# Kernel optimization log

Measured on AMD Instinct MI355X. Metric: run time of the kernel, lower is better.

The kernel has to match this reference:

```python
import jax, jax.numpy as jnp
import numpy as np
from jax import lax

N_EXPERTS = 256
N_GROUP = 8
TOPK_GROUP = 4
TOP_K = 8
AUX_ALPHA = 0.001


def setup_inputs() -> dict:
    key = jax.random.key(0)
    k1, k2 = jax.random.split(key)
    hidden_states = jax.random.normal(k1, (16384, 2048), dtype=jnp.float32)
    weight = jax.random.normal(k2, (N_EXPERTS, 2048), dtype=jnp.float32) * 0.02
    return {"hidden_states": hidden_states, "weight": weight}


def reference(hidden_states, weight):
    n_tokens = hidden_states.shape[0]
    group_size = N_EXPERTS // N_GROUP  # 32

    # gating logits: [N, E]
    logits = jnp.einsum('nh,eh->ne', hidden_states, weight)

    # group-restricted top-k: [N, G, group_size] -> top TOPK_GROUP per group
    group_logits = logits.reshape(n_tokens, N_GROUP, group_size)
    gw, gi = lax.top_k(group_logits, TOPK_GROUP)          # [N, G, tg]
    gw = gw.reshape(n_tokens, N_GROUP * TOPK_GROUP)
    gi = gi.reshape(n_tokens, N_GROUP * TOPK_GROUP)

    # global top-k over the pooled group winners
    topk_weights, ti = lax.top_k(gw, TOP_K)               # [N, K]
    selected_group = ti // TOPK_GROUP
    expert_in_group = jnp.take_along_axis(gi, ti, axis=1)
    topk_idx = selected_group * group_size + expert_in_group  # [N, K]

    # norm_topk_prob=True
    topk_weights = topk_weights / (jnp.sum(topk_weights, axis=-1, keepdims=True) + 1e-20)

    # auxiliary load-balancing loss (training path)
    expert_mask = jax.nn.one_hot(topk_idx.reshape(-1), N_EXPERTS, dtype=jnp.float32)
    expert_counts = expert_mask.mean(axis=0)              # [E]
    expert_probs = jax.nn.softmax(logits, axis=-1).mean(axis=0)  # [E]
    aux_loss = jnp.sum(expert_counts * expert_probs) * AUX_ALPHA

    return topk_idx, topk_weights, aux_loss
```

## Files before the change

kernel.cpp:

```cpp
#include <hip/hip_runtime.h>
#include <math.h>

#define NTOK 16384
#define KD   2048
#define NE   256
#define NCHUNK16 128
#define NCHUNK   64
#define CHUNK_DW 4096
#define TM 32
#define SL 257
#define SA 260

typedef float f32x2 __attribute__((ext_vector_type(2)));

__device__ __forceinline__ f32x2 pk_mul_lo(f32x2 a, f32x2 b) {
    f32x2 d;
    asm("v_pk_mul_f32 %0, %1, %2 op_sel:[0,0] op_sel_hi:[1,0]"
        : "=v"(d) : "v"(a), "v"(b));
    return d;
}
__device__ __forceinline__ f32x2 pk_mul_hi(f32x2 a, f32x2 b) {
    f32x2 d;
    asm("v_pk_mul_f32 %0, %1, %2 op_sel:[0,1] op_sel_hi:[1,1]"
        : "=v"(d) : "v"(a), "v"(b));
    return d;
}
__device__ __forceinline__ f32x2 pk_add(f32x2 a, f32x2 b) {
    f32x2 d;
    asm("v_pk_add_f32 %0, %1, %2" : "=v"(d) : "v"(a), "v"(b));
    return d;
}

__global__ __launch_bounds__(256) void transform_kernel(
    const float* __restrict__ wgt, float* __restrict__ Bt)
{
    const int c    = blockIdx.x >> 2;
    const int qt   = blockIdx.x & 3;
    const int slot = qt * 256 + threadIdx.x;
    const int s    = slot >> 6;
    const int lane = slot & 63;
    const int em   = lane >> 2;
    const int l    = lane & 3;
    const int e    = (s >> 1) * 32 + (s & 1) * 16 + em;
    const float* src = wgt + (size_t)e * KD + 16 * c + l;
    float4 v = make_float4(src[0], src[4], src[8], src[12]);
    *(float4*)(Bt + (size_t)c * CHUNK_DW + slot * 4) = v;
}

typedef __attribute__((address_space(1))) const void GV;
typedef __attribute__((address_space(3))) void LV;
__device__ __forceinline__ void gld_lds16(const float* g, float* l) {
    __builtin_amdgcn_global_load_lds((GV*)g, (LV*)l, 16, 0, 0);
}

__global__ __launch_bounds__(512, 4) void gate_kernel(
    const float* __restrict__ hid, const float* __restrict__ Bt,
    float* __restrict__ out, float* __restrict__ cnt, float* __restrict__ prb)
{
    __shared__ union { float bs[2][2 * CHUNK_DW]; float ls[TM][SL]; } sh;
    __shared__ float As2[2][4][SA];
    __shared__ float maxS[TM], sumS[TM], invS[TM];

    const int tid  = threadIdx.x;
    const int l    = tid & 3;
    const int eg   = (tid >> 2) & 31;
    const int tg   = tid >> 7;
    const int t0   = blockIdx.x * TM;
    const int lane = tid & 63;
    const int w    = tid >> 6;
    const int h    = w & 1;

    f32x2 acc2[4][8];
#pragma unroll
    for (int i = 0; i < 4; ++i)
#pragma unroll
        for (int j = 0; j < 8; ++j) acc2[i][j] = (f32x2){0.f, 0.f};

    const bool aact = (lane < 32);
    const int  at   = w * 4 + (lane >> 3);
    const int  aq   = lane & 7;
    float av[4];

    auto stageA_load = [&](int c) {
        if (aact)
            *(float4*)av = *(const float4*)(hid + (size_t)(t0 + at) * KD + 32 * c + 4 * aq);
    };
    auto stageA_write = [&](int buf) {
        if (aact) {
            const int base = (at >> 1) * 16 + aq * 2 + (at & 1);
#pragma unroll
            for (int ll = 0; ll < 4; ++ll)
                As2[buf][ll][base] = av[ll];
        }
    };
    auto stageB = [&](int c, int buf) {
        const float* src = Bt + (size_t)(2 * c) * CHUNK_DW + tid * 4;
        float* dst = &sh.bs[buf][tid * 4];
#pragma unroll
        for (int s = 0; s < 4; ++s)
            gld_lds16(src + s * 2048, dst + s * 2048);
    };

    stageA_load(0);
    stageB(0, 0);
    stageA_write(0);
    int cur = 0;

#pragma unroll 1
    for (int c = 0; c < NCHUNK; ++c) {
        __syncthreads();
        const int nxt = cur ^ 1;
        if (c + 1 < NCHUNK) { stageA_load(c + 1); stageB(c + 1, nxt); }

#pragma unroll
        for (int j16 = 0; j16 < 2; ++j16) {
            float4 a0[4], a1[4];
#pragma unroll
            for (int tp = 0; tp < 4; ++tp) {
                const float* ap = &As2[cur][l][(tg * 4 + tp) * 16 + j16 * 8];
                a0[tp] = *(const float4*)(ap);
                a1[tp] = *(const float4*)(ap + 4);
            }
#pragma unroll
            for (int j = 0; j < 8; ++j) {
                const float4 b = *(const float4*)
                    &sh.bs[cur][j16 * CHUNK_DW + ((j * 2 + h) << 8) + (lane << 2)];
                const f32x2 b01 = (f32x2){b.x, b.y};
                const f32x2 b23 = (f32x2){b.z, b.w};
#pragma unroll
                for (int tp = 0; tp < 4; ++tp) {
                    const f32x2 aQ0 = (f32x2){a0[tp].x, a0[tp].y};
                    const f32x2 aQ1 = (f32x2){a0[tp].z, a0[tp].w};
                    const f32x2 aQ2 = (f32x2){a1[tp].x, a1[tp].y};
                    const f32x2 aQ3 = (f32x2){a1[tp].z, a1[tp].w};
                    f32x2 s = acc2[tp][j];
                    s = pk_add(pk_mul_hi(aQ3, b23), s);
                    s = pk_add(pk_mul_lo(aQ2, b23), s);
                    s = pk_add(pk_mul_hi(aQ1, b01), s);
                    s = pk_add(pk_mul_lo(aQ0, b01), s);
                    acc2[tp][j] = s;
                }
            }
        }
        if (c + 1 < NCHUNK) stageA_write(nxt);
        cur = nxt;
    }

    __syncthreads();
#pragma unroll
    for (int tp = 0; tp < 4; ++tp)
#pragma unroll
        for (int j = 0; j < 8; ++j) {
            float sx = acc2[tp][j].x, sy = acc2[tp][j].y;
            sx = __fadd_rn(sx, __shfl_xor(sx, 1));
            sx = __fadd_rn(sx, __shfl_xor(sx, 2));
            sy = __fadd_rn(sy, __shfl_xor(sy, 1));
            sy = __fadd_rn(sy, __shfl_xor(sy, 2));
            if (l == 0) {
                sh.ls[tg * 8 + 2 * tp][eg + 32 * j]     = sx;
                sh.ls[tg * 8 + 2 * tp + 1][eg + 32 * j] = sy;
            }
        }
    if (tid < TM) sumS[tid] = 0.f;
    __syncthreads();

    if (tid < TM) {
        const float* lr = &sh.ls[tid][0];
        float tv[8]; int ti[8];
#pragma unroll
        for (int j = 0; j < 8; ++j) { tv[j] = -1e30f; ti[j] = 0; }
        float rowmax = -1e30f;

        auto ins8 = [&](float v, int idx) {
#pragma unroll
            for (int p = 0; p < 8; ++p) {
                if (v > tv[p]) {
#pragma unroll
                    for (int q = 7; q > p; --q) { tv[q] = tv[q - 1]; ti[q] = ti[q - 1]; }
                    tv[p] = v; ti[p] = idx;
                    break;
                }
            }
        };

#pragma unroll 1
        for (int g = 0; g < 8; ++g) {
            float v0 = -1e30f, v1 = -1e30f, v2 = -1e30f, v3 = -1e30f;
            int   i0 = 0, i1 = 0, i2 = 0, i3 = 0;
            for (int j = 0; j < 32; ++j) {
                const float v = lr[g * 32 + j];
                if (v > v0)      { v3=v2;i3=i2; v2=v1;i2=i1; v1=v0;i1=i0; v0=v;i0=j; }
                else if (v > v1) { v3=v2;i3=i2; v2=v1;i2=i1; v1=v;i1=j; }
                else if (v > v2) { v3=v2;i3=i2; v2=v;i2=j; }
                else if (v > v3) { v3=v;i3=j; }
            }
            rowmax = fmaxf(rowmax, v0);
            ins8(v0, g * 32 + i0);
            ins8(v1, g * 32 + i1);
            ins8(v2, g * 32 + i2);
            ins8(v3, g * 32 + i3);
        }

        const float s01 = __fadd_rn(tv[0], tv[1]);
        const float s23 = __fadd_rn(tv[2], tv[3]);
        const float s45 = __fadd_rn(tv[4], tv[5]);
        const float s67 = __fadd_rn(tv[6], tv[7]);
        float s = __fadd_rn(__fadd_rn(s01, s23), __fadd_rn(s45, s67));
        s = __fadd_rn(s, 1e-20f);

        const size_t tg2 = (size_t)(t0 + tid);
#pragma unroll
        for (int j = 0; j < 8; ++j) {
            out[tg2 * 8 + j]                    = (float)ti[j];
            out[(size_t)NTOK * 8 + tg2 * 8 + j] = __fdiv_rn(tv[j], s);
            atomicAdd(&cnt[ti[j]], 1.0f);
        }
        maxS[tid] = rowmax;
    }
    __syncthreads();

    {
        const int t  = tid >> 4;
        const int c0 = (tid & 15) * 16;
        const float m = maxS[t];
        float part = 0.f;
#pragma unroll
        for (int j = 0; j < 16; ++j) part += __expf(sh.ls[t][c0 + j] - m);
        atomicAdd(&sumS[t], part);
    }
    __syncthreads();
    if (tid < TM) invS[tid] = 1.0f / sumS[tid];
    __syncthreads();

    if (tid < NE) {
        float p = 0.f;
#pragma unroll
        for (int n = 0; n < TM; ++n) p += __expf(sh.ls[n][tid] - maxS[n]) * invS[n];
        atomicAdd(&prb[tid], p);
    }
}

__global__ void aux_kernel(const float* __restrict__ cnt,
                           const float* __restrict__ prb,
                           float* __restrict__ out)
{
    const int tid = threadIdx.x;
    float v = cnt[tid] * prb[tid];
#pragma unroll
    for (int off = 32; off; off >>= 1) v += __shfl_down(v, off, 64);
    __shared__ float ps[4];
    if ((tid & 63) == 0) ps[tid >> 6] = v;
    __syncthreads();
    if (tid == 0) {
        const float tot = ps[0] + ps[1] + ps[2] + ps[3];
        out[(size_t)NTOK * 8 * 2] = tot * (0.001f / (131072.0f * 16384.0f));
    }
}

extern "C" void kernel_launch(void* const* d_in, const int* in_sizes, int n_in,
                              void* d_out, int out_size, void* d_ws, size_t ws_size,
                              hipStream_t stream)
{
    (void)in_sizes; (void)n_in; (void)out_size; (void)ws_size;
    const float* hid = (const float*)d_in[0];
    const float* wgt = (const float*)d_in[1];
    float* out = (float*)d_out;
    float* cnt = (float*)d_ws;
    float* prb = cnt + NE;
    float* Bt  = prb + NE;

    hipMemsetAsync(d_ws, 0, 2 * NE * sizeof(float), stream);
    transform_kernel<<<512, 256, 0, stream>>>(wgt, Bt);
    gate_kernel<<<NTOK / TM, 512, 0, stream>>>(hid, Bt, out, cnt, prb);
    aux_kernel<<<1, 256, 0, stream>>>(cnt, prb, out);
}
```

Baseline: 493.6 us.

## Read B directly from global and stage A per-wave without block barriers

The B operand (transformed weights) is no longer staged into LDS through global_load_lds double buffers. Each wave now reads it straight from global memory or L2 in float4 loads. The A tile is staged in a per-wave private LDS region, which removes the per-chunk __syncthreads, and waves_per_eu is pinned to 4. The aim is to cut LDS traffic and block-wide synchronisation, at the cost of much more global/L2 load traffic for B and less latency hiding for it.

```diff
diff --git a/kernel.cpp b/kernel.cpp
--- a/kernel.cpp
+++ b/kernel.cpp
@@ -4,12 +4,11 @@
 #define NTOK 16384
 #define KD   2048
 #define NE   256
-#define NCHUNK16 128
-#define NCHUNK   64
+#define NCHUNK 64
 #define CHUNK_DW 4096
 #define TM 32
 #define SL 257
-#define SA 260
+#define SAW 68
 
 typedef float f32x2 __attribute__((ext_vector_type(2)));
 
@@ -47,28 +46,26 @@
     *(float4*)(Bt + (size_t)c * CHUNK_DW + slot * 4) = v;
 }
 
-typedef __attribute__((address_space(1))) const void GV;
-typedef __attribute__((address_space(3))) void LV;
-__device__ __forceinline__ void gld_lds16(const float* g, float* l) {
-    __builtin_amdgcn_global_load_lds((GV*)g, (LV*)l, 16, 0, 0);
-}
-
-__global__ __launch_bounds__(512, 4) void gate_kernel(
+__global__ __launch_bounds__(512)
+__attribute__((amdgpu_waves_per_eu(4, 4)))
+void gate_kernel(
     const float* __restrict__ hid, const float* __restrict__ Bt,
     float* __restrict__ out, float* __restrict__ cnt, float* __restrict__ prb)
 {
-    __shared__ union { float bs[2][2 * CHUNK_DW]; float ls[TM][SL]; } sh;
-    __shared__ float As2[2][4][SA];
+    __shared__ union {
+        float as[8][2][4][SAW];
+        float ls[TM][SL];
+    } sh;
     __shared__ float maxS[TM], sumS[TM], invS[TM];
 
     const int tid  = threadIdx.x;
+    const int lane = tid & 63;
+    const int w    = tid >> 6;
     const int l    = tid & 3;
     const int eg   = (tid >> 2) & 31;
     const int tg   = tid >> 7;
+    const int h    = w & 1;
     const int t0   = blockIdx.x * TM;
-    const int lane = tid & 63;
-    const int w    = tid >> 6;
-    const int h    = w & 1;
 
     f32x2 acc2[4][8];
 #pragma unroll
@@ -76,73 +73,63 @@
 #pragma unroll
         for (int j = 0; j < 8; ++j) acc2[i][j] = (f32x2){0.f, 0.f};
 
-    const bool aact = (lane < 32);
-    const int  at   = w * 4 + (lane >> 3);
-    const int  aq   = lane & 7;
-    float av[4];
-
-    auto stageA_load = [&](int c) {
-        if (aact)
-            *(float4*)av = *(const float4*)(hid + (size_t)(t0 + at) * KD + 32 * c + 4 * aq);
-    };
-    auto stageA_write = [&](int buf) {
-        if (aact) {
-            const int base = (at >> 1) * 16 + aq * 2 + (at & 1);
-#pragma unroll
-            for (int ll = 0; ll < 4; ++ll)
-                As2[buf][ll][base] = av[ll];
-        }
-    };
-    auto stageB = [&](int c, int buf) {
-        const float* src = Bt + (size_t)(2 * c) * CHUNK_DW + tid * 4;
-        float* dst = &sh.bs[buf][tid * 4];
-#pragma unroll
-        for (int s = 0; s < 4; ++s)
-            gld_lds16(src + s * 2048, dst + s * 2048);
-    };
-
-    stageA_load(0);
-    stageB(0, 0);
-    stageA_write(0);
+    const int atok = lane >> 3;
+    const int aq   = lane & 7;
+    const float* ahid = hid + (size_t)(t0 + (w >> 1) * 8 + atok) * KD + 4 * aq;
+    float* aswr = &sh.as[w][0][0][(atok >> 1) * 16 + aq * 2 + (atok & 1)];
+
+    float4 av = *(const float4*)(ahid);
+    aswr[0] = av.x; aswr[SAW] = av.y; aswr[2 * SAW] = av.z; aswr[3 * SAW] = av.w;
+    av = *(const float4*)(ahid + 32);
     int cur = 0;
 
 #pragma unroll 1
     for (int c = 0; c < NCHUNK; ++c) {
-        __syncthreads();
         const int nxt = cur ^ 1;
-        if (c + 1 < NCHUNK) { stageA_load(c + 1); stageB(c + 1, nxt); }
+        if (c + 1 < NCHUNK) {
+            float* p = aswr + nxt * (4 * SAW);
+            p[0] = av.x; p[SAW] = av.y; p[2 * SAW] = av.z; p[3 * SAW] = av.w;
+            if (c + 2 < NCHUNK) av = *(const float4*)(ahid + 32 * (c + 2));
+        }
+        const float* bc  = Bt + (size_t)c * 8192 + h * 256 + (lane << 2);
+        const float* arb = &sh.as[w][cur][l][0];
 
 #pragma unroll
         for (int j16 = 0; j16 < 2; ++j16) {
+            const float* ar = arb + j16 * 8;
             float4 a0[4], a1[4];
 #pragma unroll
             for (int tp = 0; tp < 4; ++tp) {
-                const float* ap = &As2[cur][l][(tg * 4 + tp) * 16 + j16 * 8];
-                a0[tp] = *(const float4*)(ap);
-                a1[tp] = *(const float4*)(ap + 4);
-            }
-#pragma unroll
-            for (int j = 0; j < 8; ++j) {
-                const float4 b = *(const float4*)
-                    &sh.bs[cur][j16 * CHUNK_DW + ((j * 2 + h) << 8) + (lane << 2)];
-                const f32x2 b01 = (f32x2){b.x, b.y};
-                const f32x2 b23 = (f32x2){b.z, b.w};
-#pragma unroll
-                for (int tp = 0; tp < 4; ++tp) {
-                    const f32x2 aQ0 = (f32x2){a0[tp].x, a0[tp].y};
-                    const f32x2 aQ1 = (f32x2){a0[tp].z, a0[tp].w};
-                    const f32x2 aQ2 = (f32x2){a1[tp].x, a1[tp].y};
-                    const f32x2 aQ3 = (f32x2){a1[tp].z, a1[tp].w};
-                    f32x2 s = acc2[tp][j];
-                    s = pk_add(pk_mul_hi(aQ3, b23), s);
-                    s = pk_add(pk_mul_lo(aQ2, b23), s);
-                    s = pk_add(pk_mul_hi(aQ1, b01), s);
-                    s = pk_add(pk_mul_lo(aQ0, b01), s);
-                    acc2[tp][j] = s;
+                a0[tp] = *(const float4*)(ar + tp * 16);
+                a1[tp] = *(const float4*)(ar + tp * 16 + 4);
+            }
+#pragma unroll
+            for (int jh = 0; jh < 2; ++jh) {
+                float4 b[4];
+#pragma unroll
+                for (int jj = 0; jj < 4; ++jj)
+                    b[jj] = *(const float4*)(bc + j16 * 4096 + (jh * 4 + jj) * 512);
+#pragma unroll
+                for (int jj = 0; jj < 4; ++jj) {
+                    const int j = jh * 4 + jj;
+                    const f32x2 b01 = (f32x2){b[jj].x, b[jj].y};
+                    const f32x2 b23 = (f32x2){b[jj].z, b[jj].w};
+#pragma unroll
+                    for (int tp = 0; tp < 4; ++tp) {
+                        const f32x2 aQ0 = (f32x2){a0[tp].x, a0[tp].y};
+                        const f32x2 aQ1 = (f32x2){a0[tp].z, a0[tp].w};
+                        const f32x2 aQ2 = (f32x2){a1[tp].x, a1[tp].y};
+                        const f32x2 aQ3 = (f32x2){a1[tp].z, a1[tp].w};
+                        f32x2 s = acc2[tp][j];
+                        s = pk_add(pk_mul_hi(aQ3, b23), s);
+                        s = pk_add(pk_mul_lo(aQ2, b23), s);
+                        s = pk_add(pk_mul_hi(aQ1, b01), s);
+                        s = pk_add(pk_mul_lo(aQ0, b01), s);
+                        acc2[tp][j] = s;
+                    }
                 }
             }
         }
-        if (c + 1 < NCHUNK) stageA_write(nxt);
         cur = nxt;
     }
 
```

Result: no change. 502.2 us (+1.7%).
